# Performance work log

Hardware: AMD Instinct MI355X
Metric: run time of the kernel (lower is better)

Reference implementation:

```python
import jax, jax.numpy as jnp
import numpy as np

B, C, L, H, W = 8, 512, 256, 64, 64  # batch, in_channels, latent_channels, spatial
EPS = 1e-5


def setup_inputs() -> dict:
    key = jax.random.key(0)
    ks = jax.random.split(key, 16)

    def n(k, shape, s=1.0):
        return jax.random.normal(k, shape, dtype=jnp.float32) * s

    return {
        "x_f": n(ks[0], (B, C, H, W)),
        "x_g": n(ks[1], (B, C, H, W)),
        "x_h": n(ks[2], (B, C, H, W)),
        "x_t": n(ks[3], (B, C, H, W)),
        # stacked per-stream params, stream order (f, g, h, t)
        "Wk": n(ks[4], (4, L, C), 0.02), "bk": n(ks[5], (4, L), 0.02),
        "gk": jnp.ones((4, L), jnp.float32), "betak": jnp.zeros((4, L), jnp.float32),
        "mk": n(ks[6], (4, L), 0.1),
        "vk": jax.random.uniform(ks[7], (4, L), jnp.float32, 0.5, 1.5),
        "Wq": n(ks[8], (4, L, C), 0.02), "bq": n(ks[9], (4, L), 0.02),
        "gq": jnp.ones((4, L), jnp.float32), "betaq": jnp.zeros((4, L), jnp.float32),
        "mq": n(ks[10], (4, L), 0.1),
        "vq": jax.random.uniform(ks[11], (4, L), jnp.float32, 0.5, 1.5),
        "Wd": n(ks[12], (4, L, C), 0.02), "bd": n(ks[13], (4, L), 0.02),
        "Wu": n(ks[14], (4, C, L), 0.02), "bu": n(ks[15], (4, C), 0.02),
    }


def _conv1x1(x, Wt, b):
    # x: [4,B,C,H,W], Wt: [4,L,C] -> [4,B,L,H,W]
    return jnp.einsum('sbchw,slc->sblhw', x, Wt) + b[:, None, :, None, None]


def _bn_relu(y, g, beta, m, v):
    scale = (g / jnp.sqrt(v + EPS))[:, None, :, None, None]
    return jax.nn.relu((y - m[:, None, :, None, None]) * scale + beta[:, None, :, None, None])


def reference(x_f, x_g, x_h, x_t, Wk, bk, gk, betak, mk, vk,
              Wq, bq, gq, betaq, mq, vq, Wd, bd, Wu, bu):
    x = jnp.stack([x_f, x_g, x_h, x_t])  # [4,B,C,H,W]
    b_, c_, h_, w_ = x_f.shape
    l_ = Wk.shape[1]

    k = _bn_relu(_conv1x1(x, Wk, bk), gk, betak, mk, vk)   # [4,B,L,H,W]
    q = _bn_relu(_conv1x1(x, Wq, bq), gq, betaq, mq, vq)   # [4,B,L,H,W]
    val = _conv1x1(x, Wd, bd)                              # [4,B,L,H,W]

    # faithful torch .view on contiguous NCHW: raw reshape, not transpose
    kv = k.reshape(4, b_, h_, w_, l_)
    qv = q.reshape(4, b_, h_, w_, l_)
    vv = val.reshape(4, b_, h_, w_, l_)

    q4 = jnp.moveaxis(qv, 0, 3)  # [B,H,W,4,L]  (cat dim4 then permute)
    k4 = jnp.moveaxis(kv, 0, 4)  # [B,H,W,L,4]  (cat dim4)
    v4 = jnp.moveaxis(vv, 0, 3)  # [B,H,W,4,L]

    sim = jnp.einsum('bhwsl,bhwlt->bhwst', q4, k4) * (l_ ** -0.5)  # [B,H,W,4,4]
    attn = jax.nn.softmax(sim, axis=-1)
    ctx = jnp.einsum('bhwst,bhwtl->bhwsl', attn, v4)               # [B,H,W,4,L]

    ctx = jnp.moveaxis(ctx, 3, 0)  # [4,B,H,W,L]
    up = jnp.einsum('sbhwl,scl->sbchw', ctx, Wu) + bu[:, None, :, None, None]
    out = x + up  # [4,B,C,H,W]
    return (out[0], out[1], out[2], out[3])
```

## Files before the change

kernel.cpp:

```cpp
#include <hip/hip_runtime.h>

#define B_   8
#define C_   512
#define L_   256
#define HW_  4096
#define EPSV 1e-5f

typedef short  short8   __attribute__((ext_vector_type(8)));
typedef float  floatx4  __attribute__((ext_vector_type(4)));
typedef unsigned short ushort8v __attribute__((ext_vector_type(8)));

__device__ __forceinline__ unsigned short f2bf(float f) {
    unsigned u = __float_as_uint(f);
    u = (u + 0x7FFF + ((u >> 16) & 1)) >> 16;
    return (unsigned short)u;
}
__device__ __forceinline__ float bf2f(unsigned short h) {
    return __uint_as_float(((unsigned)h) << 16);
}

#define AS3 __attribute__((address_space(3)))
#define AS1 __attribute__((address_space(1)))
__device__ __forceinline__ void async_cp16(const void* g, void* l) {
    __builtin_amdgcn_global_load_lds((const AS1 void*)g, (AS3 void*)l, 16, 0, 0);
}

__global__ __launch_bounds__(256) void prep_kernel(
    const float* __restrict__ Wk, const float* __restrict__ bk,
    const float* __restrict__ gk, const float* __restrict__ betak,
    const float* __restrict__ mk, const float* __restrict__ vk,
    const float* __restrict__ Wq, const float* __restrict__ bq,
    const float* __restrict__ gq, const float* __restrict__ betaq,
    const float* __restrict__ mq, const float* __restrict__ vq,
    const float* __restrict__ Wd, const float* __restrict__ bd,
    const float* __restrict__ Wu,
    unsigned short* __restrict__ Aall, float* __restrict__ biasA,
    unsigned short* __restrict__ Wub)
{
    const int NA = 4 * 768 * C_;
    const int NW = 4 * C_ * L_;
    const int NB = 4 * 768;
    int idx = blockIdx.x * 256 + threadIdx.x;
    if (idx < NA) {
        int s = idx / (768 * C_);
        int rem = idx % (768 * C_);
        int r = rem / C_, c = rem % C_;
        float w;
        if (r < 256) {
            int sl = s * L_ + r;
            float sc = gk[sl] * rsqrtf(vk[sl] + EPSV);
            w = Wk[(size_t)sl * C_ + c] * sc;
        } else if (r < 512) {
            int sl = s * L_ + (r - 256);
            float sc = gq[sl] * rsqrtf(vq[sl] + EPSV);
            w = Wq[(size_t)sl * C_ + c] * sc;
        } else {
            int sl = s * L_ + (r - 512);
            w = Wd[(size_t)sl * C_ + c];
        }
        Aall[idx] = f2bf(w);
    } else if (idx < NA + NW) {
        int i = idx - NA;
        Wub[i] = f2bf(Wu[i]);
    } else if (idx < NA + NW + NB) {
        int i = idx - NA - NW;
        int s = i / 768, r = i % 768;
        float bv;
        if (r < 256) {
            int sl = s * L_ + r;
            float sc = gk[sl] * rsqrtf(vk[sl] + EPSV);
            bv = (bk[sl] - mk[sl]) * sc + betak[sl];
        } else if (r < 512) {
            int sl = s * L_ + (r - 256);
            float sc = gq[sl] * rsqrtf(vq[sl] + EPSV);
            bv = (bq[sl] - mq[sl]) * sc + betaq[sl];
        } else {
            bv = bd[s * L_ + (r - 512)];
        }
        biasA[i] = bv;
    }
}

__global__ __launch_bounds__(256) void transpose_kernel(
    const float* __restrict__ xf, const float* __restrict__ xg,
    const float* __restrict__ xh, const float* __restrict__ xt,
    unsigned short* __restrict__ xT)
{
    __shared__ unsigned short tile[64][66];
    int p0 = blockIdx.x * 64;
    int c0 = blockIdx.y * 64;
    int sb = blockIdx.z;
    int s = sb >> 3, b = sb & 7;
    const float* x = (s == 0) ? xf : (s == 1) ? xg : (s == 2) ? xh : xt;
    const float* xb = x + (size_t)b * C_ * HW_;
    int tid = threadIdx.x;
    int g = tid >> 4;
    int t = tid & 15;
    int p4 = t * 4;
#pragma unroll
    for (int i = 0; i < 4; ++i) {
        int r = g + i * 16;
        float4 v = *(const float4*)&xb[(size_t)(c0 + r) * HW_ + p0 + p4];
        tile[r][p4 + 0] = f2bf(v.x);
        tile[r][p4 + 1] = f2bf(v.y);
        tile[r][p4 + 2] = f2bf(v.z);
        tile[r][p4 + 3] = f2bf(v.w);
    }
    __syncthreads();
    unsigned short* o = xT + (size_t)sb * HW_ * C_;
    int c4 = t * 4;
#pragma unroll
    for (int i = 0; i < 4; ++i) {
        int p = g + i * 16;
        ushort4 u;
        u.x = tile[c4 + 0][p];
        u.y = tile[c4 + 1][p];
        u.z = tile[c4 + 2][p];
        u.w = tile[c4 + 3][p];
        *(ushort4*)&o[(size_t)(p0 + p) * C_ + c0 + c4] = u;
    }
}

__global__ __launch_bounds__(256) void down_gemm(
    const unsigned short* __restrict__ Aall, const float* __restrict__ biasA,
    const unsigned short* __restrict__ xT,
    unsigned short* __restrict__ KQV)
{
    __shared__ unsigned short smem[16384] __attribute__((aligned(16)));
    unsigned short* At = smem;
    unsigned short* Bt = smem + 4096;
    int n0 = blockIdx.x * 128;
    int m0 = blockIdx.y * 128;
    int sb = blockIdx.z;
    int s = sb >> 3;
    int tid = threadIdx.x;
    int lane = tid & 63, wave = tid >> 6;
    int wm = (wave & 1) * 64, wn = (wave >> 1) * 64;
    int quad = lane >> 4, l16 = lane & 15;
    const unsigned short* Abase = Aall + (size_t)s * 768 * C_;
    const unsigned short* Bbase = xT + (size_t)sb * HW_ * C_;

    floatx4 acc[4][4];
#pragma unroll
    for (int i = 0; i < 4; ++i)
#pragma unroll
        for (int j = 0; j < 4; ++j) acc[i][j] = (floatx4){0.f, 0.f, 0.f, 0.f};

    for (int kt = 0; kt < C_ / 32; ++kt) {
        int k0 = kt * 32;
#pragma unroll
        for (int it = 0; it < 2; ++it) {
            int slot = tid + it * 256;
            int row  = slot >> 2;
            int pos  = slot & 3;
            int kg   = pos ^ ((row >> 1) & 3);
            async_cp16(Abase + (size_t)(m0 + row) * C_ + k0 + kg * 8, &At[slot * 8]);
            async_cp16(Bbase + (size_t)(n0 + row) * C_ + k0 + kg * 8, &Bt[slot * 8]);
        }
        __syncthreads();
        short8 a[4], bb[4];
#pragma unroll
        for (int mi = 0; mi < 4; ++mi) {
            int rr = wm + mi * 16 + l16;
            int pos = quad ^ ((rr >> 1) & 3);
            a[mi] = *(const short8*)&At[rr * 32 + pos * 8];
        }
#pragma unroll
        for (int ni = 0; ni < 4; ++ni) {
            int rr = wn + ni * 16 + l16;
            int pos = quad ^ ((rr >> 1) & 3);
            bb[ni] = *(const short8*)&Bt[rr * 32 + pos * 8];
        }
#pragma unroll
        for (int mi = 0; mi < 4; ++mi)
#pragma unroll
            for (int ni = 0; ni < 4; ++ni)
                acc[mi][ni] = __builtin_amdgcn_mfma_f32_16x16x32_bf16(
                    a[mi], bb[ni], acc[mi][ni], 0, 0, 0);
        __syncthreads();
    }

    unsigned short* Ot = smem;
#pragma unroll
    for (int mi = 0; mi < 4; ++mi) {
        int rbase = wm + mi * 16 + quad * 4;
#pragma unroll
        for (int r = 0; r < 4; ++r) {
            int row = rbase + r;
            int gm = m0 + row;
            float bias = biasA[s * 768 + gm];
            bool doRelu = (gm < 512);
#pragma unroll
            for (int ni = 0; ni < 4; ++ni) {
                int col = wn + ni * 16 + l16;
                float v = acc[mi][ni][r] + bias;
                if (doRelu) v = fmaxf(v, 0.f);
                Ot[row * 128 + col] = f2bf(v);
            }
        }
    }
    __syncthreads();
#pragma unroll
    for (int i = 0; i < 8; ++i) {
        int fo = (tid + i * 256) * 8;
        int row = fo >> 7;
        int col = fo & 127;
        *(ushort8v*)&KQV[((size_t)sb * 768 + m0 + row) * HW_ + n0 + col] =
            *(const ushort8v*)&Ot[fo];
    }
}

__global__ __launch_bounds__(256) void attn_kernel(
    const unsigned short* __restrict__ KQV, unsigned short* __restrict__ Ctx)
{
    int gw = (blockIdx.x * 256 + threadIdx.x) >> 6;
    int lane = threadIdx.x & 63;
    int b = gw >> 12;
    int j = gw & 4095;

    float qf[4][4], kf[4][4], vf[4][4];
#pragma unroll
    for (int s = 0; s < 4; ++s) {
        size_t sbase = (size_t)(s * 8 + b) * (768 * HW_) + (size_t)j * 256 + lane * 4;
        ushort4 ku = *(const ushort4*)(KQV + sbase);
        ushort4 qu = *(const ushort4*)(KQV + sbase + (size_t)256 * HW_);
        ushort4 vu = *(const ushort4*)(KQV + sbase + (size_t)512 * HW_);
        qf[s][0] = bf2f(qu.x); qf[s][1] = bf2f(qu.y); qf[s][2] = bf2f(qu.z); qf[s][3] = bf2f(qu.w);
        kf[s][0] = bf2f(ku.x); kf[s][1] = bf2f(ku.y); kf[s][2] = bf2f(ku.z); kf[s][3] = bf2f(ku.w);
        vf[s][0] = bf2f(vu.x); vf[s][1] = bf2f(vu.y); vf[s][2] = bf2f(vu.z); vf[s][3] = bf2f(vu.w);
    }
    float p[4][4];
#pragma unroll
    for (int s = 0; s < 4; ++s)
#pragma unroll
        for (int t = 0; t < 4; ++t) {
            float acc = 0.f;
#pragma unroll
            for (int e = 0; e < 4; ++e) acc += qf[s][e] * kf[t][e];
            p[s][t] = acc;
        }
#pragma unroll
    for (int off = 1; off < 64; off <<= 1)
#pragma unroll
        for (int s = 0; s < 4; ++s)
#pragma unroll
            for (int t = 0; t < 4; ++t)
                p[s][t] += __shfl_xor(p[s][t], off, 64);

    float at[4][4];
#pragma unroll
    for (int s = 0; s < 4; ++s) {
        float m = -1e30f;
#pragma unroll
        for (int t = 0; t < 4; ++t) { p[s][t] *= 0.0625f; m = fmaxf(m, p[s][t]); }
        float sm = 0.f;
#pragma unroll
        for (int t = 0; t < 4; ++t) { at[s][t] = __expf(p[s][t] - m); sm += at[s][t]; }
        float inv = 1.f / sm;
#pragma unroll
        for (int t = 0; t < 4; ++t) at[s][t] *= inv;
    }
#pragma unroll
    for (int s = 0; s < 4; ++s) {
        float c[4] = {0.f, 0.f, 0.f, 0.f};
#pragma unroll
        for (int t = 0; t < 4; ++t)
#pragma unroll
            for (int e = 0; e < 4; ++e) c[e] += at[s][t] * vf[t][e];
        ushort4 o;
        o.x = f2bf(c[0]); o.y = f2bf(c[1]); o.z = f2bf(c[2]); o.w = f2bf(c[3]);
        *(ushort4*)(Ctx + (size_t)(s * 8 + b) * (L_ * HW_) + (size_t)j * 256 + lane * 4) = o;
    }
}

__global__ __launch_bounds__(256) void up_gemm(
    const unsigned short* __restrict__ Wub, const float* __restrict__ bu,
    const unsigned short* __restrict__ Ctx,
    const float* __restrict__ xf, const float* __restrict__ xg,
    const float* __restrict__ xh, const float* __restrict__ xt,
    float* __restrict__ out)
{
    __shared__ unsigned short At[128 * 32] __attribute__((aligned(16)));
    __shared__ unsigned short Bt[128 * 32] __attribute__((aligned(16)));
    int n0 = blockIdx.x * 128;
    int m0 = blockIdx.y * 128;
    int sb = blockIdx.z;
    int s = sb >> 3, b = sb & 7;
    int tid = threadIdx.x;
    int lane = tid & 63, wave = tid >> 6;
    int wm = (wave & 1) * 64, wn = (wave >> 1) * 64;
    int quad = lane >> 4, l16 = lane & 15;
    const unsigned short* Abase = Wub + (size_t)s * C_ * L_;
    const unsigned short* Bbase = Ctx + (size_t)sb * HW_ * L_;

    floatx4 acc[4][4];
#pragma unroll
    for (int i = 0; i < 4; ++i)
#pragma unroll
        for (int j = 0; j < 4; ++j) acc[i][j] = (floatx4){0.f, 0.f, 0.f, 0.f};

    for (int kt = 0; kt < L_ / 32; ++kt) {
        int k0 = kt * 32;
#pragma unroll
        for (int it = 0; it < 2; ++it) {
            int slot = tid + it * 256;
            int row  = slot >> 2;
            int pos  = slot & 3;
            int kg   = pos ^ ((row >> 1) & 3);
            async_cp16(Abase + (size_t)(m0 + row) * L_ + k0 + kg * 8, &At[slot * 8]);
            async_cp16(Bbase + (size_t)(n0 + row) * L_ + k0 + kg * 8, &Bt[slot * 8]);
        }
        __syncthreads();
        short8 a[4], bb[4];
#pragma unroll
        for (int mi = 0; mi < 4; ++mi) {
            int rr = wm + mi * 16 + l16;
            int pos = quad ^ ((rr >> 1) & 3);
            a[mi] = *(const short8*)&At[rr * 32 + pos * 8];
        }
#pragma unroll
        for (int ni = 0; ni < 4; ++ni) {
            int rr = wn + ni * 16 + l16;
            int pos = quad ^ ((rr >> 1) & 3);
            bb[ni] = *(const short8*)&Bt[rr * 32 + pos * 8];
        }
#pragma unroll
        for (int mi = 0; mi < 4; ++mi)
#pragma unroll
            for (int ni = 0; ni < 4; ++ni)
                acc[mi][ni] = __builtin_amdgcn_mfma_f32_16x16x32_bf16(
                    a[mi], bb[ni], acc[mi][ni], 0, 0, 0);
        __syncthreads();
    }

    const float* x = (s == 0) ? xf : (s == 1) ? xg : (s == 2) ? xh : xt;
    const float* xb = x + (size_t)b * C_ * HW_;
#pragma unroll
    for (int mi = 0; mi < 4; ++mi) {
        int gmBase = m0 + wm + mi * 16 + quad * 4;
#pragma unroll
        for (int r = 0; r < 4; ++r) {
            int gm = gmBase + r;
            float bias = bu[s * C_ + gm];
#pragma unroll
            for (int ni = 0; ni < 4; ++ni) {
                int gn = n0 + wn + ni * 16 + l16;
                float rx = __builtin_nontemporal_load(&xb[(size_t)gm * HW_ + gn]);
                float v = acc[mi][ni][r] + bias + rx;
                __builtin_nontemporal_store(v, &out[((size_t)sb * C_ + gm) * HW_ + gn]);
            }
        }
    }
}

extern "C" void kernel_launch(void* const* d_in, const int* in_sizes, int n_in,
                              void* d_out, int out_size, void* d_ws, size_t ws_size,
                              hipStream_t stream) {
    (void)in_sizes; (void)n_in; (void)out_size; (void)ws_size;
    const float* xf    = (const float*)d_in[0];
    const float* xg    = (const float*)d_in[1];
    const float* xh    = (const float*)d_in[2];
    const float* xt    = (const float*)d_in[3];
    const float* Wk    = (const float*)d_in[4];
    const float* bk    = (const float*)d_in[5];
    const float* gk    = (const float*)d_in[6];
    const float* betak = (const float*)d_in[7];
    const float* mk    = (const float*)d_in[8];
    const float* vk    = (const float*)d_in[9];
    const float* Wq    = (const float*)d_in[10];
    const float* bq    = (const float*)d_in[11];
    const float* gq    = (const float*)d_in[12];
    const float* betaq = (const float*)d_in[13];
    const float* mq    = (const float*)d_in[14];
    const float* vq    = (const float*)d_in[15];
    const float* Wd    = (const float*)d_in[16];
    const float* bd    = (const float*)d_in[17];
    const float* Wu    = (const float*)d_in[18];
    const float* bu    = (const float*)d_in[19];

    char* ws = (char*)d_ws;
    unsigned short* Aall  = (unsigned short*)(ws + 0);
    float*          biasA = (float*)(ws + 3145728);
    unsigned short* Wub   = (unsigned short*)(ws + 3158016);
    unsigned short* xT    = (unsigned short*)(ws + 4206592);
    unsigned short* KQV   = (unsigned short*)(ws + 138424320);
    unsigned short* Ctx   = (unsigned short*)(ws + 339750912);

    prep_kernel<<<dim3(8204), 256, 0, stream>>>(
        Wk, bk, gk, betak, mk, vk, Wq, bq, gq, betaq, mq, vq, Wd, bd, Wu,
        Aall, biasA, Wub);
    transpose_kernel<<<dim3(64, 8, 32), 256, 0, stream>>>(xf, xg, xh, xt, xT);
    down_gemm<<<dim3(32, 6, 32), 256, 0, stream>>>(Aall, biasA, xT, KQV);
    attn_kernel<<<dim3(8192), 256, 0, stream>>>(KQV, Ctx);
    up_gemm<<<dim3(32, 4, 32), 256, 0, stream>>>(Wub, bu, Ctx, xf, xg, xh, xt,
                                                 (float*)d_out);
}
```

Before: 818.1 us.

## Double-buffer LDS tiles in down and up GEMM main loops

Both GEMM kernels now split LDS into two 16 KB-aligned buffers. Each iteration issues the async global-to-LDS copies for the next K tile before running the MFMA work on the current tile. Previously each iteration waited on its own loads right before compute. The aim is to hide global-load latency behind matrix math. up_gemm's LDS footprint doubles, which may reduce how many blocks fit per CU.

Result: no change. 806.6 us (-1.4%).

```diff
diff --git a/kernel.cpp b/kernel.cpp
--- a/kernel.cpp
+++ b/kernel.cpp
@@ -23,6 +23,25 @@
 #define AS1 __attribute__((address_space(1)))
 __device__ __forceinline__ void async_cp16(const void* g, void* l) {
     __builtin_amdgcn_global_load_lds((const AS1 void*)g, (AS3 void*)l, 16, 0, 0);
+}
+
+template<int STRIDE>
+__device__ __forceinline__ void stage_tile(
+    const unsigned short* __restrict__ Abase,
+    const unsigned short* __restrict__ Bbase,
+    unsigned short* smem, int bufBase, int tid, int m0, int n0, int k0)
+{
+#pragma unroll
+    for (int it = 0; it < 2; ++it) {
+        int slot = tid + it * 256;
+        int row  = slot >> 2;
+        int pos  = slot & 3;
+        int kg   = pos ^ ((row >> 1) & 3);
+        async_cp16(Abase + (size_t)(m0 + row) * STRIDE + k0 + kg * 8,
+                   &smem[bufBase + slot * 8]);
+        async_cp16(Bbase + (size_t)(n0 + row) * STRIDE + k0 + kg * 8,
+                   &smem[bufBase + 4096 + slot * 8]);
+    }
 }
 
 __global__ __launch_bounds__(256) void prep_kernel(
@@ -127,8 +146,6 @@
     unsigned short* __restrict__ KQV)
 {
     __shared__ unsigned short smem[16384] __attribute__((aligned(16)));
-    unsigned short* At = smem;
-    unsigned short* Bt = smem + 4096;
     int n0 = blockIdx.x * 128;
     int m0 = blockIdx.y * 128;
     int sb = blockIdx.z;
@@ -146,18 +163,17 @@
 #pragma unroll
         for (int j = 0; j < 4; ++j) acc[i][j] = (floatx4){0.f, 0.f, 0.f, 0.f};
 
+    stage_tile<C_>(Abase, Bbase, smem, 0, tid, m0, n0, 0);
+    __syncthreads();
+
+    int cur = 0;
+#pragma unroll 2
     for (int kt = 0; kt < C_ / 32; ++kt) {
-        int k0 = kt * 32;
-#pragma unroll
-        for (int it = 0; it < 2; ++it) {
-            int slot = tid + it * 256;
-            int row  = slot >> 2;
-            int pos  = slot & 3;
-            int kg   = pos ^ ((row >> 1) & 3);
-            async_cp16(Abase + (size_t)(m0 + row) * C_ + k0 + kg * 8, &At[slot * 8]);
-            async_cp16(Bbase + (size_t)(n0 + row) * C_ + k0 + kg * 8, &Bt[slot * 8]);
-        }
-        __syncthreads();
+        int nxt = cur ^ 8192;
+        if (kt + 1 < C_ / 32)
+            stage_tile<C_>(Abase, Bbase, smem, nxt, tid, m0, n0, (kt + 1) * 32);
+        const unsigned short* At = &smem[cur];
+        const unsigned short* Bt = &smem[cur + 4096];
         short8 a[4], bb[4];
 #pragma unroll
         for (int mi = 0; mi < 4; ++mi) {
@@ -178,6 +194,7 @@
                 acc[mi][ni] = __builtin_amdgcn_mfma_f32_16x16x32_bf16(
                     a[mi], bb[ni], acc[mi][ni], 0, 0, 0);
         __syncthreads();
+        cur = nxt;
     }
 
     unsigned short* Ot = smem;
@@ -280,8 +297,7 @@
     const float* __restrict__ xh, const float* __restrict__ xt,
     float* __restrict__ out)
 {
-    __shared__ unsigned short At[128 * 32] __attribute__((aligned(16)));
-    __shared__ unsigned short Bt[128 * 32] __attribute__((aligned(16)));
+    __shared__ unsigned short smem[16384] __attribute__((aligned(16)));
     int n0 = blockIdx.x * 128;
     int m0 = blockIdx.y * 128;
     int sb = blockIdx.z;
@@ -299,18 +315,17 @@
 #pragma unroll
         for (int j = 0; j < 4; ++j) acc[i][j] = (floatx4){0.f, 0.f, 0.f, 0.f};
 
+    stage_tile<L_>(Abase, Bbase, smem, 0, tid, m0, n0, 0);
+    __syncthreads();
+
+    int cur = 0;
+#pragma unroll 2
     for (int kt = 0; kt < L_ / 32; ++kt) {
-        int k0 = kt * 32;
-#pragma unroll
-        for (int it = 0; it < 2; ++it) {
-            int slot = tid + it * 256;
-            int row  = slot >> 2;
-            int pos  = slot & 3;
-            int kg   = pos ^ ((row >> 1) & 3);
-            async_cp16(Abase + (size_t)(m0 + row) * L_ + k0 + kg * 8, &At[slot * 8]);
-            async_cp16(Bbase + (size_t)(n0 + row) * L_ + k0 + kg * 8, &Bt[slot * 8]);
-        }
-        __syncthreads();
+        int nxt = cur ^ 8192;
+        if (kt + 1 < L_ / 32)
+            stage_tile<L_>(Abase, Bbase, smem, nxt, tid, m0, n0, (kt + 1) * 32);
+        const unsigned short* At = &smem[cur];
+        const unsigned short* Bt = &smem[cur + 4096];
         short8 a[4], bb[4];
 #pragma unroll
         for (int mi = 0; mi < 4; ++mi) {
@@ -331,6 +346,7 @@
                 acc[mi][ni] = __builtin_amdgcn_mfma_f32_16x16x32_bf16(
                     a[mi], bb[ni], acc[mi][ni], 0, 0, 0);
         __syncthreads();
+        cur = nxt;
     }
 
     const float* x = (s == 0) ? xf : (s == 1) ? xg : (s == 2) ? xh : xt;
```
